# Kernel tuning notes

Hardware: AMD Instinct MI355X
Metric: run time of the kernel (lower is better)

## Reference

```python
import jax, jax.numpy as jnp
import numpy as np
import math

B, N, D = 2, 192, 256

def _linear_params(key, d_in, d_out):
    kw, kb = jax.random.split(key)
    scale = 1.0 / math.sqrt(d_in)
    W = jax.random.uniform(kw, (d_out, d_in), jnp.float32, -scale, scale)
    b = jax.random.uniform(kb, (d_out,), jnp.float32, -scale, scale)
    return W, b

def setup_inputs() -> dict:
    key = jax.random.key(0)
    ks = jax.random.split(key, 7)
    Edges = jax.random.normal(ks[0], (B, N * N, D), jnp.float32)
    Wq_w, Wq_b = _linear_params(ks[1], D, D)
    Wk_w, Wk_b = _linear_params(ks[2], D, D)
    Wv_w, Wv_b = _linear_params(ks[3], D, D)
    Wb_w, Wb_b = _linear_params(ks[4], D, 1)
    Wg_w, Wg_b = _linear_params(ks[5], D, D)
    Wo_w, Wo_b = _linear_params(ks[6], D, D)
    return {"Edges": Edges, "Wq_w": Wq_w, "Wq_b": Wq_b, "Wk_w": Wk_w, "Wk_b": Wk_b,
            "Wv_w": Wv_w, "Wv_b": Wv_b, "Wb_w": Wb_w, "Wb_b": Wb_b,
            "Wg_w": Wg_w, "Wg_b": Wg_b, "Wo_w": Wo_w, "Wo_b": Wo_b}

def reference(Edges, Wq_w, Wq_b, Wk_w, Wk_b, Wv_w, Wv_b, Wb_w, Wb_b, Wg_w, Wg_b, Wo_w, Wo_b):
    # Edges: [B, N*N, D]; dropout is identity in eval mode.
    Bb, NN, Dd = Edges.shape
    n = int(round(math.sqrt(NN)))
    q = (Edges @ Wq_w.T + Wq_b).reshape(Bb, n, n, Dd)
    k = (Edges @ Wk_w.T + Wk_b).reshape(Bb, n, n, Dd)
    v = (Edges @ Wv_w.T + Wv_b).reshape(Bb, n, n, Dd)
    bmat = (Edges @ Wb_w.T + Wb_b).reshape(Bb, n, n)          # b[b,i,l]
    g = jax.nn.sigmoid(Edges @ Wg_w.T + Wg_b)                  # [B, N*N, D]
    # row attention: q(i,j) . k(i,l) ; column attention: q(i,j) . k(l,j)
    scores = (jnp.einsum('bijd,bild->bijl', q, k)
              + jnp.einsum('bijd,bljd->bijl', q, k)) / math.sqrt(Dd)
    sym_bias = bmat + jnp.swapaxes(bmat, 1, 2)                 # b[i,l] + b[l,i]
    alpha = jax.nn.softmax(scores + sym_bias[:, :, None, :], axis=-1)  # [B,n,n,n]
    # first value contraction along rows; second term matches torch's
    # transpose-free add: out2[b,i,j,d] = sum_l alpha[b,j,i,l] v[b,l,i,d]
    o1 = jnp.einsum('bijl,bild->bijd', alpha, v)
    o2 = jnp.einsum('bjil,blid->bijd', alpha, v)
    out = g * (o1 + o2).reshape(Bb, NN, Dd)
    out = jax.nn.relu(out @ Wo_w.T + Wo_b)
    return out
```

## Files before the change

### kernel.cpp

```cpp
#include <hip/hip_runtime.h>
#include <hip/hip_bf16.h>

typedef __hip_bfloat16 bf16;
typedef unsigned short u16;
typedef __attribute__((ext_vector_type(8))) short bf16x8;
typedef __attribute__((ext_vector_type(4))) float f32x4;

#define NB   2
#define NG   192
#define DD   256
#define NN2  (NG*NG)
#define MT   (NB*NN2)

static __device__ __forceinline__ float bfu2f(u16 u){
    return __uint_as_float(((unsigned)u) << 16);
}
static __device__ __forceinline__ u16 f2bfu(float f){
    bf16 h = __float2bfloat16(f);
    return *(u16*)&h;
}

static __device__ __forceinline__ void gl_lds16(const void* g, void* l){
    __builtin_amdgcn_global_load_lds(
        (const __attribute__((address_space(1))) unsigned int*)g,
        (__attribute__((address_space(3))) unsigned int*)l, 16, 0, 0);
}
static __device__ __forceinline__ int swz3(int x){ return ((x ^ (x>>3)) & 7) << 3; }

__global__ __launch_bounds__(256) void k_cast_e(const float* __restrict__ E, u16* __restrict__ Eb){
    size_t i = ((size_t)blockIdx.x*256 + threadIdx.x)*8;
    float4 x = *(const float4*)(E+i);
    float4 y = *(const float4*)(E+i+4);
    ushort4 a; a.x=f2bfu(x.x); a.y=f2bfu(x.y); a.z=f2bfu(x.z); a.w=f2bfu(x.w);
    ushort4 b; b.x=f2bfu(y.x); b.y=f2bfu(y.y); b.z=f2bfu(y.z); b.w=f2bfu(y.w);
    *(ushort4*)(Eb+i)   = a;
    *(ushort4*)(Eb+i+4) = b;
}

__global__ __launch_bounds__(256) void k_cast_w(
    const float* __restrict__ Wq, const float* __restrict__ Wk,
    const float* __restrict__ Wv, const float* __restrict__ Wg,
    const float* __restrict__ Wo, const float* __restrict__ Wb,
    const float* __restrict__ bq, const float* __restrict__ bk,
    const float* __restrict__ bv, const float* __restrict__ bg,
    u16* __restrict__ Wcat, u16* __restrict__ Wob, u16* __restrict__ Wbb,
    float* __restrict__ biascat)
{
    int e = blockIdx.x*256 + threadIdx.x;
    Wcat[e]          = f2bfu(Wq[e]);
    Wcat[65536 + e]  = f2bfu(Wk[e]);
    Wcat[131072 + e] = f2bfu(Wv[e]);
    Wcat[196608 + e] = f2bfu(Wg[e]);
    Wob[e]           = f2bfu(Wo[e]);
    if (e < 256) Wbb[e] = f2bfu(Wb[e]);
    if (e < 1024){
        int p = e>>8, r = e&255;
        const float* bp = p==0?bq : p==1?bk : p==2?bv : bg;
        biascat[e] = bp[r];
    }
}

static __device__ __forceinline__ void gemm128_acc(
    const u16* __restrict__ A, size_t Ast,
    const u16* __restrict__ B, size_t Bst,
    u16* As, u16* Bs, f32x4 acc[4][4], int t)
{
    const int lane = t & 63, w = t >> 6;
    const int wm = (w>>1)*64, wn = (w&1)*64;
    int offA[4], offB[4];
    #pragma unroll
    for (int f=0; f<4; f++){
        int ra = wm + f*16 + (lane&15);
        offA[f] = ra*32 + (((lane>>4) ^ ((ra>>1)&3)) << 3);
        int rb = wn + f*16 + (lane&15);
        offB[f] = rb*32 + (((lane>>4) ^ ((rb>>1)&3)) << 3);
    }
    for (int k0=0; k0<DD; k0+=32){
        #pragma unroll
        for (int it=0; it<2; it++){
            int c = it*256 + t;
            int row = c >> 2;
            int ks  = (c&3) ^ ((row>>1)&3);
            gl_lds16(A + (size_t)row*Ast + k0 + ks*8, As + c*8);
            gl_lds16(B + (size_t)row*Bst + k0 + ks*8, Bs + c*8);
        }
        __syncthreads();
        bf16x8 a[4], b[4];
        #pragma unroll
        for (int f=0; f<4; f++) a[f] = *(const bf16x8*)(As + offA[f]);
        #pragma unroll
        for (int f=0; f<4; f++) b[f] = *(const bf16x8*)(Bs + offB[f]);
        #pragma unroll
        for (int mf=0; mf<4; mf++)
            #pragma unroll
            for (int nf=0; nf<4; nf++)
                acc[mf][nf] = __builtin_amdgcn_mfma_f32_16x16x32_bf16(a[mf], b[nf], acc[mf][nf], 0, 0, 0);
        __syncthreads();
    }
}

__global__ __launch_bounds__(256) void k_proj_mfma(
    const u16* __restrict__ Eb, const u16* __restrict__ Wcat,
    const float* __restrict__ biascat,
    u16* __restrict__ qb, u16* __restrict__ kb,
    u16* __restrict__ vb, u16* __restrict__ gb)
{
    __shared__ u16 As[128*32];
    __shared__ u16 Bs[128*32];
    const int m0 = blockIdx.x*128, n0 = blockIdx.y*128;
    const int t = threadIdx.x, lane = t&63, w = t>>6;
    f32x4 acc[4][4];
    #pragma unroll
    for (int i=0;i<4;i++)
        #pragma unroll
        for (int j=0;j<4;j++) acc[i][j] = f32x4{0.f,0.f,0.f,0.f};
    gemm128_acc(Eb + (size_t)m0*DD, DD, Wcat + (size_t)n0*DD, DD, As, Bs, acc, t);

    const int p = n0 >> 8;
    u16* outp = p==0?qb : p==1?kb : p==2?vb : gb;
    const int wm = (w>>1)*64, wn = (w&1)*64;
    #pragma unroll
    for (int mf=0; mf<4; mf++){
        int m = m0 + wm + mf*16 + (lane>>4)*4;
        #pragma unroll
        for (int nf=0; nf<4; nf++){
            int gn = n0 + wn + nf*16 + (lane&15);
            float bias = biascat[gn];
            int col = gn & 255;
            #pragma unroll
            for (int r=0; r<4; r++){
                float v = acc[mf][nf][r] + bias;
                if (p==3) v = 1.0f/(1.0f+__expf(-v));
                outp[(size_t)(m+r)*DD + col] = f2bfu(v);
            }
        }
    }
}

__global__ __launch_bounds__(256) void k_final_mfma(
    const u16* __restrict__ hb, const u16* __restrict__ Wob,
    const float* __restrict__ bo, float* __restrict__ out)
{
    __shared__ u16 As[128*32];
    __shared__ u16 Bs[128*32];
    const int m0 = blockIdx.x*128, n0 = blockIdx.y*128;
    const int t = threadIdx.x, lane = t&63, w = t>>6;
    f32x4 acc[4][4];
    #pragma unroll
    for (int i=0;i<4;i++)
        #pragma unroll
        for (int j=0;j<4;j++) acc[i][j] = f32x4{0.f,0.f,0.f,0.f};
    gemm128_acc(hb + (size_t)m0*DD, DD, Wob + (size_t)n0*DD, DD, As, Bs, acc, t);

    const int wm = (w>>1)*64, wn = (w&1)*64;
    #pragma unroll
    for (int mf=0; mf<4; mf++){
        int m = m0 + wm + mf*16 + (lane>>4)*4;
        #pragma unroll
        for (int nf=0; nf<4; nf++){
            int n = n0 + wn + nf*16 + (lane&15);
            float bias = bo[n];
            #pragma unroll
            for (int r=0; r<4; r++)
                out[(size_t)(m+r)*DD + n] = fmaxf(acc[mf][nf][r] + bias, 0.0f);
        }
    }
}

__global__ __launch_bounds__(256) void k_bmat(
    const u16* __restrict__ Eb, const u16* __restrict__ Wbb,
    const float* __restrict__ bb, float* __restrict__ bm)
{
    int row = blockIdx.x*8 + (threadIdx.x >> 5);
    int l32 = threadIdx.x & 31;
    const u16* er = Eb + (size_t)row*DD + l32*8;
    const u16* wr = Wbb + l32*8;
    float s = 0.f;
    #pragma unroll
    for (int q=0; q<8; q++) s += bfu2f(er[q]) * bfu2f(wr[q]);
    #pragma unroll
    for (int off=16; off; off>>=1) s += __shfl_xor(s, off);
    if (l32 == 0) bm[row] = s + bb[0];
}

__global__ __launch_bounds__(256) void k_bias_sym(
    const float* __restrict__ bm, float* __restrict__ biassym)
{
    int rem = blockIdx.x*256 + threadIdx.x;
    int b = blockIdx.y;
    int i = rem / NG, l = rem % NG;
    biassym[(size_t)b*NN2 + rem] = bm[(size_t)b*NN2 + rem] + bm[(size_t)b*NN2 + l*NG + i];
}

template<int MODE>
__global__ __launch_bounds__(512, 2) void k_scores(
    const u16* __restrict__ q, const u16* __restrict__ kmat,
    const float* __restrict__ biassym, float* __restrict__ scores)
{
    __shared__ u16 As[2][NG*64];
    __shared__ u16 Bs[2][NG*64];
    const int z = blockIdx.x, b = z/NG, r = z%NG;
    const int t = threadIdx.x, lane = t&63, w = t>>6;
    const int wm = (w&3)*48, wn = (w>>2)*96;
    const size_t astr = MODE ? (size_t)NG*DD : (size_t)DD;
    const u16* Ab = MODE ? q    + ((size_t)b*NN2 + r)*DD : q    + ((size_t)b*NG + r)*NG*DD;
    const u16* Bb = MODE ? kmat + ((size_t)b*NN2 + r)*DD : kmat + ((size_t)b*NG + r)*NG*DD;

    f32x4 acc[3][6];
    #pragma unroll
    for (int i=0;i<3;i++)
        #pragma unroll
        for (int j=0;j<6;j++) acc[i][j] = f32x4{0.f,0.f,0.f,0.f};

    int offA[3], offB[6];
    #pragma unroll
    for (int mf=0; mf<3; mf++){
        int x = wm + mf*16 + (lane&15);
        offA[mf] = x*64 + (((lane>>4)<<3) ^ swz3(x));
    }
    #pragma unroll
    for (int nf=0; nf<6; nf++){
        int x = wn + nf*16 + (lane&15);
        offB[nf] = x*64 + (((lane>>4)<<3) ^ swz3(x));
    }

    auto stage = [&](int buf, int k0){
        #pragma unroll
        for (int rr=0; rr<3; rr++){
            int c = t + rr*512;
            int x = c>>3, l8e = (c&7)<<3;
            size_t ro = (size_t)x*astr + k0;
            gl_lds16(Ab + ro + (l8e ^ swz3(x)), &As[buf][c*8]);
            gl_lds16(Bb + ro + (l8e ^ swz3(x)), &Bs[buf][c*8]);
        }
    };

    stage(0, 0);
    for (int ks=0; ks<4; ks++){
        if (ks<3){
            stage((ks+1)&1, (ks+1)*64);
            asm volatile("s_waitcnt vmcnt(6)" ::: "memory");
        } else {
            asm volatile("s_waitcnt vmcnt(0)" ::: "memory");
        }
        __builtin_amdgcn_s_barrier();
        const u16* A = &As[ks&1][0];
        const u16* B = &Bs[ks&1][0];
        #pragma unroll
        for (int kk=0; kk<2; kk++){
            bf16x8 a[3];
            #pragma unroll
            for (int mf=0; mf<3; mf++) a[mf] = *(const bf16x8*)(A + (offA[mf]^(kk<<5)));
            #pragma unroll
            for (int nf=0; nf<6; nf++){
                bf16x8 bf = *(const bf16x8*)(B + (offB[nf]^(kk<<5)));
                #pragma unroll
                for (int mf=0; mf<3; mf++)
                    acc[mf][nf] = __builtin_amdgcn_mfma_f32_16x16x32_bf16(a[mf], bf, acc[mf][nf], 0, 0, 0);
            }
        }
        __builtin_amdgcn_s_barrier();
    }

    const size_t base_b = (size_t)b*NN2*NG;
    #pragma unroll
    for (int mf=0; mf<3; mf++){
        #pragma unroll
        for (int nf=0; nf<6; nf++){
            int lcol = wn + nf*16 + (lane&15);
            float bias = MODE ? 0.f : biassym[((size_t)b*NG + r)*NG + lcol];
            #pragma unroll
            for (int r4=0; r4<4; r4++){
                int x = wm + mf*16 + (lane>>4)*4 + r4;
                size_t idx = MODE ? base_b + ((size_t)x*NG + r)*NG + lcol
                                  : base_b + ((size_t)r*NG + x)*NG + lcol;
                float v = acc[mf][nf][r4]*0.0625f;
                if (MODE) scores[idx] += v;
                else      scores[idx] = v + bias;
            }
        }
    }
}

__global__ __launch_bounds__(256) void k_softmax(
    const float* __restrict__ scores, u16* __restrict__ alpha, u16* __restrict__ alphaT)
{
    int rr   = blockIdx.x*4 + (threadIdx.x >> 6);
    int lane = threadIdx.x & 63;
    int b = blockIdx.y;
    int i = rr / NG, j = rr % NG;
    const float* arow = scores + ((size_t)b*NN2 + rr)*NG;
    float vals[3];
    float mx = -1e30f;
    #pragma unroll
    for (int tt=0; tt<3; tt++){
        float s = arow[lane + tt*64];
        vals[tt] = s;
        mx = fmaxf(mx, s);
    }
    #pragma unroll
    for (int off=32; off; off>>=1) mx = fmaxf(mx, __shfl_xor(mx, off));
    float sum = 0.f;
    #pragma unroll
    for (int tt=0; tt<3; tt++){ vals[tt] = __expf(vals[tt]-mx); sum += vals[tt]; }
    #pragma unroll
    for (int off=32; off; off>>=1) sum += __shfl_xor(sum, off);
    float inv = 1.0f/sum;
    u16* arow1 = alpha  + ((size_t)b*NN2 + rr)*NG;
    u16* arow2 = alphaT + ((size_t)b*NN2 + (size_t)j*NG + i)*NG;
    #pragma unroll
    for (int tt=0; tt<3; tt++){
        u16 vq = f2bfu(vals[tt]*inv);
        arow1[lane + tt*64] = vq;
        arow2[lane + tt*64] = vq;
    }
}

__global__ __launch_bounds__(512, 4) void k_attnout(
    const u16* __restrict__ alpha, const u16* __restrict__ alphaT,
    const u16* __restrict__ vb, const u16* __restrict__ gb, u16* __restrict__ hb)
{
    __shared__ u16 AsL[2][NG*64];
    __shared__ u16 Vs[128*64];
    const int z = blockIdx.x, bi = z>>1, dh = z&1;
    const int b = bi/NG, i = bi%NG;
    const int dbase = dh*128;
    const int t = threadIdx.x, lane = t&63, w = t>>6;
    const int wm = (w&1)*96, wn = (w>>1)*32;

    const u16* Abase0 = alpha  + (size_t)bi*NN2;
    const u16* Abase1 = alphaT + (size_t)bi*NN2;
    const u16* V0 = vb + (size_t)bi*NG*DD + dbase;
    const u16* V1 = vb + ((size_t)b*NG*NG + i)*DD + dbase;

    f32x4 acc[6][2];
    #pragma unroll
    for (int m=0;m<6;m++)
        #pragma unroll
        for (int n=0;n<2;n++) acc[m][n] = f32x4{0.f,0.f,0.f,0.f};

    int offA[6], offB[2];
    #pragma unroll
    for (int mf=0; mf<6; mf++){
        int j = wm + mf*16 + (lane&15);
        offA[mf] = j*64 + (((lane>>4)<<3) ^ swz3(j));
    }
    #pragma unroll
    for (int nf=0; nf<2; nf++){
        int d = wn + nf*16 + (lane&15);
        offB[nf] = d*64 + (((lane>>4)<<3) ^ swz3(d));
    }

    int4 vr[2];
    auto stageA = [&](int u, int buf){
        const u16* Ab = (u>=3) ? Abase1 : Abase0;
        int ls = (u>=3 ? u-3 : u)*64;
        #pragma unroll
        for (int rr=0; rr<3; rr++){
            int c = t + rr*512;
            int j = c>>3, l8e = (c&7)<<3;
            gl_lds16(Ab + (size_t)j*NG + ls + (l8e ^ swz3(j)), &AsL[buf][c*8]);
        }
    };
    auto loadV = [&](int u){
        int p = (u>=3), ls = (u>=3 ? u-3 : u)*64;
        #pragma unroll
        for (int rr=0; rr<2; rr++){
            int c = t + rr*512;
            int l = ls + (c>>4), d0 = (c&15)*8;
            const u16* src = p ? (V1 + (size_t)l*NG*DD + d0) : (V0 + (size_t)l*DD + d0);
            vr[rr] = *(const int4*)src;
        }
    };

    stageA(0, 0);
    loadV(0);
    for (int u=0; u<6; u++){
        #pragma unroll
        for (int rr=0; rr<2; rr++){
            int c = t + rr*512;
            int l = c>>4;
            l &= 63;
            int d0 = (c&15)*8, c3 = c&7;
            ushort* vp = (ushort*)&vr[rr];
            #pragma unroll
            for (int qd=0; qd<8; qd++)
                Vs[(d0+qd)*64 + (l ^ ((qd^c3)<<3))] = vp[qd];
        }
        if (u<5){ stageA(u+1, (u+1)&1); loadV(u+1); }
        asm volatile("s_waitcnt lgkmcnt(0)" ::: "memory");
        __builtin_amdgcn_s_barrier();
        const u16* A = &AsL[u&1][0];
        #pragma unroll
        for (int kk=0; kk<2; kk++){
            bf16x8 bfr[2];
            #pragma unroll
            for (int nf=0; nf<2; nf++) bfr[nf] = *(const bf16x8*)(Vs + (offB[nf]^(kk<<5)));
            #pragma unroll
            for (int mf=0; mf<6; mf++){
                bf16x8 afr = *(const bf16x8*)(A + (offA[mf]^(kk<<5)));
                acc[mf][0] = __builtin_amdgcn_mfma_f32_16x16x32_bf16(afr, bfr[0], acc[mf][0], 0, 0, 0);
                acc[mf][1] = __builtin_amdgcn_mfma_f32_16x16x32_bf16(afr, bfr[1], acc[mf][1], 0, 0, 0);
            }
        }
        __builtin_amdgcn_s_barrier();
    }

    #pragma unroll
    for (int mf=0; mf<6; mf++){
        #pragma unroll
        for (int nf=0; nf<2; nf++){
            #pragma unroll
            for (int r4=0; r4<4; r4++){
                int j = wm + mf*16 + (lane>>4)*4 + r4;
                int d = dbase + wn + nf*16 + (lane&15);
                size_t idx = ((size_t)bi*NG + j)*DD + d;
                hb[idx] = f2bfu(bfu2f(gb[idx]) * acc[mf][nf][r4]);
            }
        }
    }
}

extern "C" void kernel_launch(void* const* d_in, const int* in_sizes, int n_in,
                              void* d_out, int out_size, void* d_ws, size_t ws_size,
                              hipStream_t stream)
{
    const float* E  = (const float*)d_in[0];
    const float* Wq = (const float*)d_in[1];  const float* bq = (const float*)d_in[2];
    const float* Wk = (const float*)d_in[3];  const float* bk = (const float*)d_in[4];
    const float* Wv = (const float*)d_in[5];  const float* bv = (const float*)d_in[6];
    const float* Wb = (const float*)d_in[7];  const float* bb = (const float*)d_in[8];
    const float* Wg = (const float*)d_in[9];  const float* bg = (const float*)d_in[10];
    const float* Wo = (const float*)d_in[11]; const float* bo = (const float*)d_in[12];
    float* out = (float*)d_out;

    const size_t BF = (size_t)MT*DD*2;
    const size_t SC = (size_t)NB*NG*NG*NG*4;
    char* ws = (char*)d_ws;
    float* scores = (float*)ws;
    u16*   Eb     = (u16*)ws;
    u16*   hb     = (u16*)ws;
    u16* qb = (u16*)(ws + SC);           u16* alpha  = qb;
    u16* kb = (u16*)(ws + SC + BF);      u16* alphaT = kb;
    u16* vb = (u16*)(ws + SC + 2*BF);
    u16* gb = (u16*)(ws + SC + 3*BF);
    size_t tail = SC + 4*BF;
    float* bm      = (float*)(ws + tail); tail += (size_t)MT*4;
    float* biassym = (float*)(ws + tail); tail += (size_t)MT*4;
    u16* Wcat      = (u16*)(ws + tail);   tail += (size_t)1024*DD*2;
    u16* Wob       = (u16*)(ws + tail);   tail += (size_t)DD*DD*2;
    u16* Wbb       = (u16*)(ws + tail);   tail += (size_t)DD*2;
    float* biascat = (float*)(ws + tail); tail += 1024*4;
    (void)ws_size;

    k_cast_w   <<<dim3(256), 256, 0, stream>>>(Wq,Wk,Wv,Wg,Wo,Wb, bq,bk,bv,bg, Wcat, Wob, Wbb, biascat);
    k_cast_e   <<<dim3(9216), 256, 0, stream>>>(E, Eb);
    k_proj_mfma<<<dim3(MT/128, 8), 256, 0, stream>>>(Eb, Wcat, biascat, qb, kb, vb, gb);
    k_bmat     <<<dim3(MT/8), 256, 0, stream>>>(Eb, Wbb, bb, bm);
    k_bias_sym <<<dim3(NN2/256, NB), 256, 0, stream>>>(bm, biassym);
    k_scores<0><<<dim3(NB*NG), 512, 0, stream>>>(qb, kb, biassym, scores);
    k_scores<1><<<dim3(NB*NG), 512, 0, stream>>>(qb, kb, biassym, scores);
    k_softmax  <<<dim3(NN2/4, NB), 256, 0, stream>>>(scores, alpha, alphaT);
    k_attnout  <<<dim3(NB*NG*2), 512, 0, stream>>>(alpha, alphaT, vb, gb, hb);
    k_final_mfma<<<dim3(MT/128, DD/128), 256, 0, stream>>>(hb, Wob, bo, out);
}
```

Before: 278.5 us.

## Store scores as bf16 halves, fuse bias matvec into cast, double-buffer GEMMs

Measured after the change: 237.8 us. -14.6%, faster.

```diff
diff --git a/kernel.cpp b/kernel.cpp
--- a/kernel.cpp
+++ b/kernel.cpp
@@ -27,24 +27,35 @@
 }
 static __device__ __forceinline__ int swz3(int x){ return ((x ^ (x>>3)) & 7) << 3; }
 
-__global__ __launch_bounds__(256) void k_cast_e(const float* __restrict__ E, u16* __restrict__ Eb){
-    size_t i = ((size_t)blockIdx.x*256 + threadIdx.x)*8;
-    float4 x = *(const float4*)(E+i);
-    float4 y = *(const float4*)(E+i+4);
+__global__ __launch_bounds__(256) void k_cast_eb(
+    const float* __restrict__ E, const float* __restrict__ Wb,
+    const float* __restrict__ bb, u16* __restrict__ Eb, float* __restrict__ bm)
+{
+    const int t = threadIdx.x;
+    size_t base = (size_t)blockIdx.x*2048 + t*8;
+    float4 x = *(const float4*)(E+base);
+    float4 y = *(const float4*)(E+base+4);
     ushort4 a; a.x=f2bfu(x.x); a.y=f2bfu(x.y); a.z=f2bfu(x.z); a.w=f2bfu(x.w);
     ushort4 b; b.x=f2bfu(y.x); b.y=f2bfu(y.y); b.z=f2bfu(y.z); b.w=f2bfu(y.w);
-    *(ushort4*)(Eb+i)   = a;
-    *(ushort4*)(Eb+i+4) = b;
+    *(ushort4*)(Eb+base)   = a;
+    *(ushort4*)(Eb+base+4) = b;
+    const int l32 = t & 31;
+    float4 w0 = ((const float4*)Wb)[l32*2];
+    float4 w1 = ((const float4*)Wb)[l32*2+1];
+    float s = x.x*w0.x + x.y*w0.y + x.z*w0.z + x.w*w0.w
+            + y.x*w1.x + y.y*w1.y + y.z*w1.z + y.w*w1.w;
+    #pragma unroll
+    for (int off=1; off<32; off<<=1) s += __shfl_xor(s, off);
+    if (l32 == 0) bm[blockIdx.x*8 + (t>>5)] = s + bb[0];
 }
 
 __global__ __launch_bounds__(256) void k_cast_w(
     const float* __restrict__ Wq, const float* __restrict__ Wk,
     const float* __restrict__ Wv, const float* __restrict__ Wg,
-    const float* __restrict__ Wo, const float* __restrict__ Wb,
+    const float* __restrict__ Wo,
     const float* __restrict__ bq, const float* __restrict__ bk,
     const float* __restrict__ bv, const float* __restrict__ bg,
-    u16* __restrict__ Wcat, u16* __restrict__ Wob, u16* __restrict__ Wbb,
-    float* __restrict__ biascat)
+    u16* __restrict__ Wcat, u16* __restrict__ Wob, float* __restrict__ biascat)
 {
     int e = blockIdx.x*256 + threadIdx.x;
     Wcat[e]          = f2bfu(Wq[e]);
@@ -52,7 +63,6 @@
     Wcat[131072 + e] = f2bfu(Wv[e]);
     Wcat[196608 + e] = f2bfu(Wg[e]);
     Wob[e]           = f2bfu(Wo[e]);
-    if (e < 256) Wbb[e] = f2bfu(Wb[e]);
     if (e < 1024){
         int p = e>>8, r = e&255;
         const float* bp = p==0?bq : p==1?bk : p==2?bv : bg;
@@ -60,9 +70,17 @@
     }
 }
 
-static __device__ __forceinline__ void gemm128_acc(
-    const u16* __restrict__ A, size_t Ast,
-    const u16* __restrict__ B, size_t Bst,
+__global__ __launch_bounds__(256) void k_bias_sym(
+    const float* __restrict__ bm, float* __restrict__ biassym)
+{
+    int rem = blockIdx.x*256 + threadIdx.x;
+    int b = blockIdx.y;
+    int i = rem / NG, l = rem % NG;
+    biassym[(size_t)b*NN2 + rem] = bm[(size_t)b*NN2 + rem] + bm[(size_t)b*NN2 + l*NG + i];
+}
+
+static __device__ __forceinline__ void gemm128_dbuf(
+    const u16* __restrict__ A, const u16* __restrict__ B,
     u16* As, u16* Bs, f32x4 acc[4][4], int t)
 {
     const int lane = t & 63, w = t >> 6;
@@ -75,27 +93,38 @@
         int rb = wn + f*16 + (lane&15);
         offB[f] = rb*32 + (((lane>>4) ^ ((rb>>1)&3)) << 3);
     }
-    for (int k0=0; k0<DD; k0+=32){
+    auto stage = [&](int buf, int k0){
         #pragma unroll
         for (int it=0; it<2; it++){
             int c = it*256 + t;
             int row = c >> 2;
             int ks  = (c&3) ^ ((row>>1)&3);
-            gl_lds16(A + (size_t)row*Ast + k0 + ks*8, As + c*8);
-            gl_lds16(B + (size_t)row*Bst + k0 + ks*8, Bs + c*8);
-        }
-        __syncthreads();
+            gl_lds16(A + (size_t)row*DD + k0 + ks*8, As + buf*4096 + c*8);
+            gl_lds16(B + (size_t)row*DD + k0 + ks*8, Bs + buf*4096 + c*8);
+        }
+    };
+    stage(0, 0);
+    for (int ks=0; ks<8; ks++){
+        if (ks<7){
+            stage((ks+1)&1, (ks+1)*32);
+            asm volatile("s_waitcnt vmcnt(4)" ::: "memory");
+        } else {
+            asm volatile("s_waitcnt vmcnt(0)" ::: "memory");
+        }
+        __builtin_amdgcn_s_barrier();
+        const u16* Ab = As + (ks&1)*4096;
+        const u16* Bb = Bs + (ks&1)*4096;
         bf16x8 a[4], b[4];
         #pragma unroll
-        for (int f=0; f<4; f++) a[f] = *(const bf16x8*)(As + offA[f]);
-        #pragma unroll
-        for (int f=0; f<4; f++) b[f] = *(const bf16x8*)(Bs + offB[f]);
+        for (int f=0; f<4; f++) a[f] = *(const bf16x8*)(Ab + offA[f]);
+        #pragma unroll
+        for (int f=0; f<4; f++) b[f] = *(const bf16x8*)(Bb + offB[f]);
         #pragma unroll
         for (int mf=0; mf<4; mf++)
             #pragma unroll
             for (int nf=0; nf<4; nf++)
                 acc[mf][nf] = __builtin_amdgcn_mfma_f32_16x16x32_bf16(a[mf], b[nf], acc[mf][nf], 0, 0, 0);
-        __syncthreads();
+        __builtin_amdgcn_s_barrier();
     }
 }
 
@@ -105,16 +134,19 @@
     u16* __restrict__ qb, u16* __restrict__ kb,
     u16* __restrict__ vb, u16* __restrict__ gb)
 {
-    __shared__ u16 As[128*32];
-    __shared__ u16 Bs[128*32];
-    const int m0 = blockIdx.x*128, n0 = blockIdx.y*128;
+    __shared__ u16 As[2*4096];
+    __shared__ u16 Bs[2*4096];
+    const int blk = blockIdx.x;
+    const int xj = blk & 7, xi = blk >> 3;
+    const int m0 = (xj*72 + (xi>>3)) * 128;
+    const int n0 = (xi & 7) * 128;
     const int t = threadIdx.x, lane = t&63, w = t>>6;
     f32x4 acc[4][4];
     #pragma unroll
     for (int i=0;i<4;i++)
         #pragma unroll
         for (int j=0;j<4;j++) acc[i][j] = f32x4{0.f,0.f,0.f,0.f};
-    gemm128_acc(Eb + (size_t)m0*DD, DD, Wcat + (size_t)n0*DD, DD, As, Bs, acc, t);
+    gemm128_dbuf(Eb + (size_t)m0*DD, Wcat + (size_t)n0*DD, As, Bs, acc, t);
 
     const int p = n0 >> 8;
     u16* outp = p==0?qb : p==1?kb : p==2?vb : gb;
@@ -141,16 +173,19 @@
     const u16* __restrict__ hb, const u16* __restrict__ Wob,
     const float* __restrict__ bo, float* __restrict__ out)
 {
-    __shared__ u16 As[128*32];
-    __shared__ u16 Bs[128*32];
-    const int m0 = blockIdx.x*128, n0 = blockIdx.y*128;
+    __shared__ u16 As[2*4096];
+    __shared__ u16 Bs[2*4096];
+    const int blk = blockIdx.x;
+    const int xj = blk & 7, xi = blk >> 3;
+    const int m0 = (xj*72 + (xi>>1)) * 128;
+    const int n0 = (xi & 1) * 128;
     const int t = threadIdx.x, lane = t&63, w = t>>6;
     f32x4 acc[4][4];
     #pragma unroll
     for (int i=0;i<4;i++)
         #pragma unroll
         for (int j=0;j<4;j++) acc[i][j] = f32x4{0.f,0.f,0.f,0.f};
-    gemm128_acc(hb + (size_t)m0*DD, DD, Wob + (size_t)n0*DD, DD, As, Bs, acc, t);
+    gemm128_dbuf(hb + (size_t)m0*DD, Wob + (size_t)n0*DD, As, Bs, acc, t);
 
     const int wm = (w>>1)*64, wn = (w&1)*64;
     #pragma unroll
@@ -167,35 +202,10 @@
     }
 }
 
-__global__ __launch_bounds__(256) void k_bmat(
-    const u16* __restrict__ Eb, const u16* __restrict__ Wbb,
-    const float* __restrict__ bb, float* __restrict__ bm)
-{
-    int row = blockIdx.x*8 + (threadIdx.x >> 5);
-    int l32 = threadIdx.x & 31;
-    const u16* er = Eb + (size_t)row*DD + l32*8;
-    const u16* wr = Wbb + l32*8;
-    float s = 0.f;
-    #pragma unroll
-    for (int q=0; q<8; q++) s += bfu2f(er[q]) * bfu2f(wr[q]);
-    #pragma unroll
-    for (int off=16; off; off>>=1) s += __shfl_xor(s, off);
-    if (l32 == 0) bm[row] = s + bb[0];
-}
-
-__global__ __launch_bounds__(256) void k_bias_sym(
-    const float* __restrict__ bm, float* __restrict__ biassym)
-{
-    int rem = blockIdx.x*256 + threadIdx.x;
-    int b = blockIdx.y;
-    int i = rem / NG, l = rem % NG;
-    biassym[(size_t)b*NN2 + rem] = bm[(size_t)b*NN2 + rem] + bm[(size_t)b*NN2 + l*NG + i];
-}
-
 template<int MODE>
 __global__ __launch_bounds__(512, 2) void k_scores(
     const u16* __restrict__ q, const u16* __restrict__ kmat,
-    const float* __restrict__ biassym, float* __restrict__ scores)
+    u16* __restrict__ outS)
 {
     __shared__ u16 As[2][NG*64];
     __shared__ u16 Bs[2][NG*64];
@@ -262,39 +272,39 @@
         __builtin_amdgcn_s_barrier();
     }
 
-    const size_t base_b = (size_t)b*NN2*NG;
+    u16* outb = outS + ((size_t)b*NG + r)*NN2;
     #pragma unroll
     for (int mf=0; mf<3; mf++){
         #pragma unroll
         for (int nf=0; nf<6; nf++){
             int lcol = wn + nf*16 + (lane&15);
-            float bias = MODE ? 0.f : biassym[((size_t)b*NG + r)*NG + lcol];
             #pragma unroll
             for (int r4=0; r4<4; r4++){
                 int x = wm + mf*16 + (lane>>4)*4 + r4;
-                size_t idx = MODE ? base_b + ((size_t)x*NG + r)*NG + lcol
-                                  : base_b + ((size_t)r*NG + x)*NG + lcol;
-                float v = acc[mf][nf][r4]*0.0625f;
-                if (MODE) scores[idx] += v;
-                else      scores[idx] = v + bias;
+                outb[(size_t)x*NG + lcol] = f2bfu(acc[mf][nf][r4]*0.0625f);
             }
         }
     }
 }
 
 __global__ __launch_bounds__(256) void k_softmax(
-    const float* __restrict__ scores, u16* __restrict__ alpha, u16* __restrict__ alphaT)
+    const u16* __restrict__ S1, const u16* __restrict__ S2T,
+    const float* __restrict__ biassym,
+    u16* __restrict__ alpha, u16* __restrict__ alphaT)
 {
     int rr   = blockIdx.x*4 + (threadIdx.x >> 6);
     int lane = threadIdx.x & 63;
     int b = blockIdx.y;
     int i = rr / NG, j = rr % NG;
-    const float* arow = scores + ((size_t)b*NN2 + rr)*NG;
+    const u16* r1 = S1  + ((size_t)b*NN2 + rr)*NG;
+    const u16* r2 = S2T + ((size_t)b*NN2 + (size_t)j*NG + i)*NG;
+    const float* bs = biassym + ((size_t)b*NG + i)*NG;
     float vals[3];
     float mx = -1e30f;
     #pragma unroll
     for (int tt=0; tt<3; tt++){
-        float s = arow[lane + tt*64];
+        int l = lane + tt*64;
+        float s = bfu2f(r1[l]) + bfu2f(r2[l]) + bs[l];
         vals[tt] = s;
         mx = fmaxf(mx, s);
     }
@@ -437,9 +447,10 @@
     const size_t BF = (size_t)MT*DD*2;
     const size_t SC = (size_t)NB*NG*NG*NG*4;
     char* ws = (char*)d_ws;
-    float* scores = (float*)ws;
-    u16*   Eb     = (u16*)ws;
-    u16*   hb     = (u16*)ws;
+    u16* Eb  = (u16*)ws;
+    u16* S1  = (u16*)ws;
+    u16* S2T = (u16*)(ws + SC/2);
+    u16* hb  = (u16*)ws;
     u16* qb = (u16*)(ws + SC);           u16* alpha  = qb;
     u16* kb = (u16*)(ws + SC + BF);      u16* alphaT = kb;
     u16* vb = (u16*)(ws + SC + 2*BF);
@@ -449,18 +460,16 @@
     float* biassym = (float*)(ws + tail); tail += (size_t)MT*4;
     u16* Wcat      = (u16*)(ws + tail);   tail += (size_t)1024*DD*2;
     u16* Wob       = (u16*)(ws + tail);   tail += (size_t)DD*DD*2;
-    u16* Wbb       = (u16*)(ws + tail);   tail += (size_t)DD*2;
     float* biascat = (float*)(ws + tail); tail += 1024*4;
     (void)ws_size;
 
-    k_cast_w   <<<dim3(256), 256, 0, stream>>>(Wq,Wk,Wv,Wg,Wo,Wb, bq,bk,bv,bg, Wcat, Wob, Wbb, biascat);
-    k_cast_e   <<<dim3(9216), 256, 0, stream>>>(E, Eb);
-    k_proj_mfma<<<dim3(MT/128, 8), 256, 0, stream>>>(Eb, Wcat, biascat, qb, kb, vb, gb);
-    k_bmat     <<<dim3(MT/8), 256, 0, stream>>>(Eb, Wbb, bb, bm);
+    k_cast_w   <<<dim3(256), 256, 0, stream>>>(Wq,Wk,Wv,Wg,Wo, bq,bk,bv,bg, Wcat, Wob, biascat);
+    k_cast_eb  <<<dim3(9216), 256, 0, stream>>>(E, Wb, bb, Eb, bm);
+    k_proj_mfma<<<dim3(4608), 256, 0, stream>>>(Eb, Wcat, biascat, qb, kb, vb, gb);
     k_bias_sym <<<dim3(NN2/256, NB), 256, 0, stream>>>(bm, biassym);
-    k_scores<0><<<dim3(NB*NG), 512, 0, stream>>>(qb, kb, biassym, scores);
-    k_scores<1><<<dim3(NB*NG), 512, 0, stream>>>(qb, kb, biassym, scores);
-    k_softmax  <<<dim3(NN2/4, NB), 256, 0, stream>>>(scores, alpha, alphaT);
+    k_scores<0><<<dim3(NB*NG), 512, 0, stream>>>(qb, kb, S1);
+    k_scores<1><<<dim3(NB*NG), 512, 0, stream>>>(qb, kb, S2T);
+    k_softmax  <<<dim3(NN2/4, NB), 256, 0, stream>>>(S1, S2T, biassym, alpha, alphaT);
     k_attnout  <<<dim3(NB*NG*2), 512, 0, stream>>>(alpha, alphaT, vb, gb, hb);
-    k_final_mfma<<<dim3(MT/128, DD/128), 256, 0, stream>>>(hb, Wob, bo, out);
-}
+    k_final_mfma<<<dim3(1152), 256, 0, stream>>>(hb, Wob, bo, out);
+}
```
